# Performance work log

Hardware: AMD Instinct MI355X
Metric: run time of the kernel (lower is better)

Reference implementation:

```python
import jax, jax.numpy as jnp
import numpy as np


def sinusoidal_pe(S, D, dtype):
    # standard transformer sinusoidal positional encoding, shape [S, D]
    pos = jnp.arange(S, dtype=jnp.float32)[:, None]
    div = jnp.exp(jnp.arange(0, D, 2, dtype=jnp.float32) * (-np.log(10000.0) / D))
    ang = pos * div  # [S, D/2]
    pe = jnp.zeros((S, D), jnp.float32)
    pe = pe.at[:, 0::2].set(jnp.sin(ang)).at[:, 1::2].set(jnp.cos(ang))
    return pe.astype(dtype)


def setup_inputs() -> dict:
    key = jax.random.key(0)
    k1, k2, k3, k4, k5 = jax.random.split(key, 5)
    B, S, F, D, SEG = 64, 512, 64, 1024, 8
    x = jax.random.normal(k1, (B, S, F), jnp.float32)
    W_emb = jax.random.normal(k2, (F, D), jnp.float32) / np.sqrt(F)
    b_emb = jax.random.normal(k3, (D,), jnp.float32) * 0.01
    w_seg = jax.random.normal(k4, (SEG,), jnp.float32) / np.sqrt(SEG)
    b_seg = jax.random.normal(k5, (1,), jnp.float32) * 0.01
    return {"x": x, "W_emb": W_emb, "b_emb": b_emb, "w_seg": w_seg, "b_seg": b_seg}


def reference(x, W_emb, b_emb, w_seg, b_seg):
    B, S, F = x.shape
    D = W_emb.shape[1]
    seg_len = w_seg.shape[0]  # seq_len divisible by seg_len -> pad_len == 0 branch
    # input token embedding
    x1 = x @ W_emb + b_emb  # [B, S, D]
    # segment embedding: tensor_split at multiples of seg_len == reshape,
    # Linear(seg_len, 1) over the time axis of each chunk, broadcast over chunk.
    xr = x1.reshape(B, S // seg_len, seg_len, D)
    seg = jnp.einsum('bnsd,s->bnd', xr, w_seg) + b_seg[0]  # [B, n_seg, D]
    x2 = (xr + seg[:, :, None, :]).reshape(B, S, D)
    # positional encoding added to x2
    return x2 + sinusoidal_pe(S, D, x2.dtype)
```

## Files before the change

### kernel.cpp

```cpp
#include <hip/hip_runtime.h>
#include <stdint.h>


typedef __attribute__((ext_vector_type(8))) short short8;
typedef __attribute__((ext_vector_type(4))) float f32x4;

#define D_DIM 1024
#define WS_X_OFF 131072

__device__ __forceinline__ unsigned short f2bf(float f) {
  unsigned u = __float_as_uint(f);
  u = (u + 0x7FFFu + ((u >> 16) & 1u)) >> 16;
  return (unsigned short)u;
}

__global__ __launch_bounds__(256) void bert_setup(
    const float* __restrict__ x, const float* __restrict__ W,
    unsigned short* __restrict__ wsW, unsigned short* __restrict__ wsX) {
  const int bid = blockIdx.x;
  const int tid = threadIdx.x;
  if (bid < 1024) {
    const int t = bid * 256 + tid;
    const float4* p = reinterpret_cast<const float4*>(x) + (size_t)t * 2;
    float4 v0 = p[0], v1 = p[1];
    short8 o;
    o[0] = (short)f2bf(v0.x); o[1] = (short)f2bf(v0.y);
    o[2] = (short)f2bf(v0.z); o[3] = (short)f2bf(v0.w);
    o[4] = (short)f2bf(v1.x); o[5] = (short)f2bf(v1.y);
    o[6] = (short)f2bf(v1.z); o[7] = (short)f2bf(v1.w);
    *reinterpret_cast<short8*>(wsX + (size_t)t * 8) = o;
  } else {
    const int t = (bid - 1024) * 256 + tid;
    const int cfg = t >> 7;
    const int kf = (t >> 6) & 1;
    const int lane = t & 63;
    const int col = cfg * 16 + (lane & 15);
    const int k0 = kf * 32 + ((lane >> 4) << 3);
    short8 o;
#pragma unroll
    for (int i = 0; i < 8; ++i)
      o[i] = (short)f2bf(W[(size_t)(k0 + i) * D_DIM + col]);
    *reinterpret_cast<short8*>(wsW + (size_t)t * 8) = o;
  }
}

__global__ __launch_bounds__(256) void bert_main(
    const unsigned short* __restrict__ wsX,
    const unsigned short* __restrict__ wsW, const float* __restrict__ b_emb,
    const float* __restrict__ w_seg, const float* __restrict__ b_seg,
    float* __restrict__ out) {
  const int tid = threadIdx.x;
  const int lane = tid & 63;
  const int wave = tid >> 6;
  const int bid = blockIdx.x;
  const int nblk = (bid >> 3) & 7;
  const int mblk = (bid & 7) | ((bid >> 6) << 3);
  const int mbase = mblk * 64;
  const int nbase = nblk * 128;
  const int mw = wave >> 1;
  const int nw = wave & 1;
  const int L15 = lane & 15;
  const int g = lane >> 4;

  short8 aW[4][2];
#pragma unroll
  for (int cf = 0; cf < 4; ++cf)
#pragma unroll
    for (int kf = 0; kf < 2; ++kf) {
      const int cfg = (nbase >> 4) + nw * 4 + cf;
      aW[cf][kf] = *reinterpret_cast<const short8*>(
          wsW + ((size_t)(cfg * 2 + kf) * 64 + lane) * 8);
    }

  short8 bX[2][2];
#pragma unroll
  for (int rf = 0; rf < 2; ++rf)
#pragma unroll
    for (int kf = 0; kf < 2; ++kf) {
      const int row = mbase + mw * 32 + rf * 16 + L15;
      bX[rf][kf] = *reinterpret_cast<const short8*>(
          wsX + (size_t)row * 64 + kf * 32 + g * 8);
    }

  f32x4 acc[4][2];
#pragma unroll
  for (int cf = 0; cf < 4; ++cf)
#pragma unroll
    for (int rf = 0; rf < 2; ++rf) {
      f32x4 c = {0.f, 0.f, 0.f, 0.f};
      c = __builtin_amdgcn_mfma_f32_16x16x32_bf16(aW[cf][0], bX[rf][0], c, 0, 0, 0);
      c = __builtin_amdgcn_mfma_f32_16x16x32_bf16(aW[cf][1], bX[rf][1], c, 0, 0, 0);
      acc[cf][rf] = c;
    }

  float Sw = 0.f;
#pragma unroll
  for (int i = 0; i < 8; ++i) Sw += w_seg[i];
  const float s1w = 1.f + Sw;
  const float bseg = b_seg[0];
  const float tseg = w_seg[lane & 7];

  const float inv2pi = 0.15915494309189535f;
  const float KLOG = 0.02595256324130752f;
  float dv[4][2];
#pragma unroll
  for (int cf = 0; cf < 4; ++cf) {
    const int p = (nbase + nw * 64 + cf * 16 + g * 4) >> 1;
    dv[cf][0] = exp2f(-(float)p * KLOG) * inv2pi;
    dv[cf][1] = exp2f(-(float)(p + 1) * KLOG) * inv2pi;
  }

#pragma unroll
  for (int cf = 0; cf < 4; ++cf) {
    const int colq = nbase + nw * 64 + cf * 16 + g * 4;
    const float4 eb = *reinterpret_cast<const float4*>(b_emb + colq);
    const float e0 = eb.x * s1w + bseg, e1 = eb.y * s1w + bseg;
    const float e2 = eb.z * s1w + bseg, e3 = eb.w * s1w + bseg;
#pragma unroll
    for (int rf = 0; rf < 2; ++rf) {
      f32x4 a = acc[cf][rf];
      float q0 = a[0] * tseg, q1 = a[1] * tseg, q2 = a[2] * tseg, q3 = a[3] * tseg;
      q0 += __shfl_xor(q0, 1); q1 += __shfl_xor(q1, 1);
      q2 += __shfl_xor(q2, 1); q3 += __shfl_xor(q3, 1);
      q0 += __shfl_xor(q0, 2); q1 += __shfl_xor(q1, 2);
      q2 += __shfl_xor(q2, 2); q3 += __shfl_xor(q3, 2);
      q0 += __shfl_xor(q0, 4); q1 += __shfl_xor(q1, 4);
      q2 += __shfl_xor(q2, 4); q3 += __shfl_xor(q3, 4);

      const int row = mbase + mw * 32 + rf * 16 + L15;
      const float s = (float)(row & 511);
      const float pe0 = __builtin_amdgcn_sinf(__builtin_amdgcn_fractf(s * dv[cf][0]));
      const float pe1 = __builtin_amdgcn_sinf(__builtin_amdgcn_fractf(s * dv[cf][0] + 0.25f));
      const float pe2 = __builtin_amdgcn_sinf(__builtin_amdgcn_fractf(s * dv[cf][1]));
      const float pe3 = __builtin_amdgcn_sinf(__builtin_amdgcn_fractf(s * dv[cf][1] + 0.25f));

      float4 o;
      o.x = a[0] + q0 + pe0 + e0;
      o.y = a[1] + q1 + pe1 + e1;
      o.z = a[2] + q2 + pe2 + e2;
      o.w = a[3] + q3 + pe3 + e3;
      *reinterpret_cast<float4*>(out + (size_t)row * D_DIM + colq) = o;
    }
  }
}

extern "C" void kernel_launch(void* const* d_in, const int* in_sizes, int n_in,
                              void* d_out, int out_size, void* d_ws,
                              size_t ws_size, hipStream_t stream) {
  const float* x = (const float*)d_in[0];
  const float* W = (const float*)d_in[1];
  const float* b_emb = (const float*)d_in[2];
  const float* w_seg = (const float*)d_in[3];
  const float* b_seg = (const float*)d_in[4];
  float* out = (float*)d_out;

  unsigned short* wsW = (unsigned short*)d_ws;
  unsigned short* wsX = (unsigned short*)((char*)d_ws + WS_X_OFF);

  bert_setup<<<1056, 256, 0, stream>>>(x, W, wsW, wsX);
  bert_main<<<4096, 256, 0, stream>>>(wsX, wsW, b_emb, w_seg, b_seg, out);
}
```

Baseline: 39.38 us.

## Fold segment mixing into input prep and precompute PE+bias table

The segment-linear term is moved ahead of the GEMM: since the segment mix is linear, it is applied to x (mixing the 8 rows of each segment) before bf16 conversion, which removes the cross-lane shuffle reduction from the GEMM epilogue. The setup kernel also precomputes a [512,1024] fp32 table holding the positional encoding plus the folded bias terms, so the main kernel's epilogue becomes a load and an add instead of sin evaluations. This trades transcendental and shuffle work for an extra 2 MB table written once and read repeatedly, mostly from cache. Rounding changes slightly because the segment sum is now computed before bf16 quantization.

```diff
diff --git a/kernel.cpp b/kernel.cpp
--- a/kernel.cpp
+++ b/kernel.cpp
@@ -4,9 +4,11 @@
 
 typedef __attribute__((ext_vector_type(8))) short short8;
 typedef __attribute__((ext_vector_type(4))) float f32x4;
+typedef __attribute__((ext_vector_type(4))) unsigned short u16x4;
 
 #define D_DIM 1024
-#define WS_X_OFF 131072
+#define WS_PE_OFF 131072
+#define WS_X_OFF (131072 + 2097152)
 
 __device__ __forceinline__ unsigned short f2bf(float f) {
   unsigned u = __float_as_uint(f);
@@ -16,21 +18,57 @@
 
 __global__ __launch_bounds__(256) void bert_setup(
     const float* __restrict__ x, const float* __restrict__ W,
-    unsigned short* __restrict__ wsW, unsigned short* __restrict__ wsX) {
+    const float* __restrict__ b_emb, const float* __restrict__ w_seg,
+    const float* __restrict__ b_seg, unsigned short* __restrict__ wsW,
+    float* __restrict__ wsPE, unsigned short* __restrict__ wsX) {
   const int bid = blockIdx.x;
   const int tid = threadIdx.x;
   if (bid < 1024) {
-    const int t = bid * 256 + tid;
-    const float4* p = reinterpret_cast<const float4*>(x) + (size_t)t * 2;
-    float4 v0 = p[0], v1 = p[1];
-    short8 o;
-    o[0] = (short)f2bf(v0.x); o[1] = (short)f2bf(v0.y);
-    o[2] = (short)f2bf(v0.z); o[3] = (short)f2bf(v0.w);
-    o[4] = (short)f2bf(v1.x); o[5] = (short)f2bf(v1.y);
-    o[6] = (short)f2bf(v1.z); o[7] = (short)f2bf(v1.w);
-    *reinterpret_cast<short8*>(wsX + (size_t)t * 8) = o;
+    const int lane = tid & 63;
+    const int gg = bid * 4 + (tid >> 6);
+    const size_t base = (size_t)gg * 512;
+    const int sl = lane >> 4;
+    const int c0 = (lane & 15) * 4;
+    const float4 v1 = *reinterpret_cast<const float4*>(x + base + lane * 4);
+    const float4 v2 = *reinterpret_cast<const float4*>(x + base + 256 + lane * 4);
+    const float wa = w_seg[sl], wb = w_seg[sl + 4];
+    float q0 = wa * v1.x + wb * v2.x;
+    float q1 = wa * v1.y + wb * v2.y;
+    float q2 = wa * v1.z + wb * v2.z;
+    float q3 = wa * v1.w + wb * v2.w;
+    q0 += __shfl_xor(q0, 16); q1 += __shfl_xor(q1, 16);
+    q2 += __shfl_xor(q2, 16); q3 += __shfl_xor(q3, 16);
+    q0 += __shfl_xor(q0, 32); q1 += __shfl_xor(q1, 32);
+    q2 += __shfl_xor(q2, 32); q3 += __shfl_xor(q3, 32);
+    u16x4 o1, o2;
+    o1[0] = f2bf(v1.x + q0); o1[1] = f2bf(v1.y + q1);
+    o1[2] = f2bf(v1.z + q2); o1[3] = f2bf(v1.w + q3);
+    o2[0] = f2bf(v2.x + q0); o2[1] = f2bf(v2.y + q1);
+    o2[2] = f2bf(v2.z + q2); o2[3] = f2bf(v2.w + q3);
+    *reinterpret_cast<u16x4*>(wsX + base + sl * 64 + c0) = o1;
+    *reinterpret_cast<u16x4*>(wsX + base + (sl + 4) * 64 + c0) = o2;
+  } else if (bid < 1536) {
+    const int t = (bid - 1024) * 256 + tid;
+    const int s = t >> 8;
+    const int c0 = (t & 255) * 4;
+    float Sw = 0.f;
+#pragma unroll
+    for (int i = 0; i < 8; ++i) Sw += w_seg[i];
+    const float inv2pi = 0.15915494309189535f;
+    const float KLOG = 0.02595256324130752f;
+    const float d0 = exp2f(-(float)(c0 >> 1) * KLOG) * inv2pi;
+    const float d1 = exp2f(-(float)((c0 >> 1) + 1) * KLOG) * inv2pi;
+    const float fs = (float)s;
+    const float4 eb = *reinterpret_cast<const float4*>(b_emb + c0);
+    const float cb = b_seg[0];
+    float4 pv;
+    pv.x = __builtin_amdgcn_sinf(__builtin_amdgcn_fractf(fs * d0)) + eb.x * (1.f + Sw) + cb;
+    pv.y = __builtin_amdgcn_sinf(__builtin_amdgcn_fractf(fs * d0 + 0.25f)) + eb.y * (1.f + Sw) + cb;
+    pv.z = __builtin_amdgcn_sinf(__builtin_amdgcn_fractf(fs * d1)) + eb.z * (1.f + Sw) + cb;
+    pv.w = __builtin_amdgcn_sinf(__builtin_amdgcn_fractf(fs * d1 + 0.25f)) + eb.w * (1.f + Sw) + cb;
+    *reinterpret_cast<float4*>(wsPE + (size_t)t * 4) = pv;
   } else {
-    const int t = (bid - 1024) * 256 + tid;
+    const int t = (bid - 1536) * 256 + tid;
     const int cfg = t >> 7;
     const int kf = (t >> 6) & 1;
     const int lane = t & 63;
@@ -46,8 +84,7 @@
 
 __global__ __launch_bounds__(256) void bert_main(
     const unsigned short* __restrict__ wsX,
-    const unsigned short* __restrict__ wsW, const float* __restrict__ b_emb,
-    const float* __restrict__ w_seg, const float* __restrict__ b_seg,
+    const unsigned short* __restrict__ wsW, const float* __restrict__ wsPE,
     float* __restrict__ out) {
   const int tid = threadIdx.x;
   const int lane = tid & 63;
@@ -93,52 +130,20 @@
       acc[cf][rf] = c;
     }
 
-  float Sw = 0.f;
-#pragma unroll
-  for (int i = 0; i < 8; ++i) Sw += w_seg[i];
-  const float s1w = 1.f + Sw;
-  const float bseg = b_seg[0];
-  const float tseg = w_seg[lane & 7];
-
-  const float inv2pi = 0.15915494309189535f;
-  const float KLOG = 0.02595256324130752f;
-  float dv[4][2];
-#pragma unroll
-  for (int cf = 0; cf < 4; ++cf) {
-    const int p = (nbase + nw * 64 + cf * 16 + g * 4) >> 1;
-    dv[cf][0] = exp2f(-(float)p * KLOG) * inv2pi;
-    dv[cf][1] = exp2f(-(float)(p + 1) * KLOG) * inv2pi;
-  }
-
 #pragma unroll
   for (int cf = 0; cf < 4; ++cf) {
     const int colq = nbase + nw * 64 + cf * 16 + g * 4;
-    const float4 eb = *reinterpret_cast<const float4*>(b_emb + colq);
-    const float e0 = eb.x * s1w + bseg, e1 = eb.y * s1w + bseg;
-    const float e2 = eb.z * s1w + bseg, e3 = eb.w * s1w + bseg;
 #pragma unroll
     for (int rf = 0; rf < 2; ++rf) {
-      f32x4 a = acc[cf][rf];
-      float q0 = a[0] * tseg, q1 = a[1] * tseg, q2 = a[2] * tseg, q3 = a[3] * tseg;
-      q0 += __shfl_xor(q0, 1); q1 += __shfl_xor(q1, 1);
-      q2 += __shfl_xor(q2, 1); q3 += __shfl_xor(q3, 1);
-      q0 += __shfl_xor(q0, 2); q1 += __shfl_xor(q1, 2);
-      q2 += __shfl_xor(q2, 2); q3 += __shfl_xor(q3, 2);
-      q0 += __shfl_xor(q0, 4); q1 += __shfl_xor(q1, 4);
-      q2 += __shfl_xor(q2, 4); q3 += __shfl_xor(q3, 4);
-
       const int row = mbase + mw * 32 + rf * 16 + L15;
-      const float s = (float)(row & 511);
-      const float pe0 = __builtin_amdgcn_sinf(__builtin_amdgcn_fractf(s * dv[cf][0]));
-      const float pe1 = __builtin_amdgcn_sinf(__builtin_amdgcn_fractf(s * dv[cf][0] + 0.25f));
-      const float pe2 = __builtin_amdgcn_sinf(__builtin_amdgcn_fractf(s * dv[cf][1]));
-      const float pe3 = __builtin_amdgcn_sinf(__builtin_amdgcn_fractf(s * dv[cf][1] + 0.25f));
-
+      const f32x4 a = acc[cf][rf];
+      const float4 pe = *reinterpret_cast<const float4*>(
+          wsPE + (size_t)(row & 511) * D_DIM + colq);
       float4 o;
-      o.x = a[0] + q0 + pe0 + e0;
-      o.y = a[1] + q1 + pe1 + e1;
-      o.z = a[2] + q2 + pe2 + e2;
-      o.w = a[3] + q3 + pe3 + e3;
+      o.x = a[0] + pe.x;
+      o.y = a[1] + pe.y;
+      o.z = a[2] + pe.z;
+      o.w = a[3] + pe.w;
       *reinterpret_cast<float4*>(out + (size_t)row * D_DIM + colq) = o;
     }
   }
@@ -155,8 +160,9 @@
   float* out = (float*)d_out;
 
   unsigned short* wsW = (unsigned short*)d_ws;
+  float* wsPE = (float*)((char*)d_ws + WS_PE_OFF);
   unsigned short* wsX = (unsigned short*)((char*)d_ws + WS_X_OFF);
 
-  bert_setup<<<1056, 256, 0, stream>>>(x, W, wsW, wsX);
-  bert_main<<<4096, 256, 0, stream>>>(wsX, wsW, b_emb, w_seg, b_seg, out);
+  bert_setup<<<1568, 256, 0, stream>>>(x, W, b_emb, w_seg, b_seg, wsW, wsPE, wsX);
+  bert_main<<<4096, 256, 0, stream>>>(wsX, wsW, wsPE, out);
 }
```

Result: slower. 48.59 us (+23.4%).
